# Kernel optimization log

Hardware: AMD Instinct MI355X
Metric: run time of the kernel (lower is better)

## Reference

```python
import jax, jax.numpy as jnp
import numpy as np
from math import factorial

N_ATOM = 32768
NODE_DIM = 128
HID = 64
MUL = 16          # hidden multiplicity per irrep
INS = [(0,0,0),(0,2,2),(1,1,0),(1,1,1),(1,1,2),(2,0,2),(2,2,0),(2,2,1),(2,2,2)]  # (l1,l2,l_out)
W_NUMEL = len(INS)*MUL*MUL  # 2304 per-sample tp weights

# ---------- real Clebsch-Gordan coefficients (e3nn-style, Frobenius-normalized) ----------
def _su2_cg(j1,j2,j3,m1,m2,m3):
    if m3 != m1+m2 or not (abs(j1-j2) <= j3 <= j1+j2):
        return 0.0
    f = factorial
    pref = np.sqrt((2*j3+1)*f(j3+j1-j2)*f(j3-j1+j2)*f(j1+j2-j3)/f(j1+j2+j3+1))
    pref *= np.sqrt(f(j3+m3)*f(j3-m3)*f(j1-m1)*f(j1+m1)*f(j2-m2)*f(j2+m2))
    s = 0.0
    for v in range(max(0, j2-j3-m1, j1-j3+m2), min(j1+j2-j3, j1-m1, j2+m2)+1):
        s += (-1)**v/(f(v)*f(j1+j2-j3-v)*f(j1-m1-v)*f(j2+m2-v)*f(j3-j2+m1+v)*f(j3-j1-m2+v))
    return pref*s

def _r2c(l):
    q = np.zeros((2*l+1,2*l+1), dtype=complex)
    for m in range(-l, 0):
        q[l+m, l+abs(m)] = 1/np.sqrt(2); q[l+m, l-abs(m)] = -1j/np.sqrt(2)
    q[l, l] = 1.0
    for m in range(1, l+1):
        q[l+m, l+abs(m)] = (-1)**m/np.sqrt(2); q[l+m, l-abs(m)] = 1j*(-1)**m/np.sqrt(2)
    return (-1j)**l * q

def real_cg(l1, l2, l3):
    C = np.zeros((2*l1+1,2*l2+1,2*l3+1), dtype=complex)
    for m1 in range(-l1, l1+1):
        for m2 in range(-l2, l2+1):
            m3 = m1+m2
            if abs(m3) <= l3:
                C[l1+m1, l2+m2, l3+m3] = _su2_cg(l1,l2,l3,m1,m2,m3)
    Cr = np.einsum('ij,kl,nm,ikn->jlm', _r2c(l1), _r2c(l2), np.conj(_r2c(l3)), C)
    re, im = np.real(Cr), np.imag(Cr)
    out = re if np.linalg.norm(re) >= np.linalg.norm(im) else im
    return (out / np.linalg.norm(out)).astype(np.float32)

_CG = {ins: real_cg(*ins) for ins in set(INS)}
# change of basis: irreps 1x0e+1x1e+1x2e (dim 9) -> cartesian 3x3 rank-2 tensor
_QF = np.concatenate([np.sqrt(2*l+1)*real_cg(l,1,1) for l in range(3)], 0).reshape(9,9).astype(np.float32)
_PERM = np.array([2,0,1])  # e3nn (y,z,x) -> cartesian (x,y,z)


def setup_inputs() -> dict:
    key = jax.random.key(0)
    ks = jax.random.split(key, 12)
    n = lambda k, s: jax.random.normal(k, s, dtype=jnp.float32)
    return {
        "x_scalar": n(ks[0], (N_ATOM, NODE_DIM)),
        "x_spherical": n(ks[1], (N_ATOM, 128 + 64*3 + 32*5)),
        "w_pre0": n(ks[2], (128, MUL)),
        "w_pre1": n(ks[3], (64, MUL)),
        "w_pre2": n(ks[4], (32, MUL)),
        "gw1": n(ks[5], (NODE_DIM, HID)) / float(np.sqrt(NODE_DIM)),
        "gb1": jnp.zeros((HID,), jnp.float32),
        "gw2": n(ks[6], (HID, W_NUMEL)) / float(np.sqrt(HID)),
        "gb2": jnp.zeros((W_NUMEL,), jnp.float32),
        "wpost0": n(ks[7], (3*MUL, 1)),
        "wpost1": n(ks[8], (2*MUL, 1)),
        "wpost2": n(ks[9], (4*MUL, 1)),
    }


def reference(x_scalar, x_spherical, w_pre0, w_pre1, w_pre2, gw1, gb1, gw2, gb2, wpost0, wpost1, wpost2):
    N = x_scalar.shape[0]
    # split edge irreps 128x0e + 64x1o + 32x2e
    x0 = x_spherical[:, :128]
    x1 = x_spherical[:, 128:320].reshape(N, 64, 3)
    x2 = x_spherical[:, 320:].reshape(N, 32, 5)
    # pre o3.Linear (per-l channel mixing, fan-in normalized)
    h = [
        (x0 @ w_pre0)[:, :, None] / float(np.sqrt(128.0)),              # [N,16,1] 0e
        jnp.einsum('num,uv->nvm', x1, w_pre1) / float(np.sqrt(64.0)),    # [N,16,3] 1o
        jnp.einsum('num,uv->nvm', x2, w_pre2) / float(np.sqrt(32.0)),    # [N,16,5] 2e
    ]
    # gate MLP -> per-sample tp weights [N, n_ins, u, w]
    g = (jax.nn.silu(x_scalar @ gw1 + gb1) @ gw2 + gb2).reshape(N, len(INS), MUL, MUL)
    # 'uuw' CG tensor product
    outs = {0: [], 1: [], 2: []}
    inv_sqrt_mul = float(1.0 / np.sqrt(MUL))
    for idx, (i, j, lo) in enumerate(INS):
        C = jnp.asarray(_CG[(i, j, lo)])
        o = jnp.einsum('nuw,abm,nua,nub->nwm', g[:, idx], C, h[i], h[j]) * inv_sqrt_mul
        outs[lo].append(o)
    # post o3.Linear: (48x0e + 32x1e + 64x2e) -> 1x0e + 1x1e + 1x2e
    wpost = [wpost0, wpost1, wpost2]
    ys = []
    for lo in range(3):
        z = jnp.concatenate(outs[lo], axis=1)                       # [N, n_paths*MUL, 2lo+1]
        y = jnp.einsum('num,uv->nvm', z, wpost[lo]) / float(np.sqrt(z.shape[1]))
        ys.append(y.reshape(N, 2*lo+1))
    atom_out = jnp.concatenate(ys, axis=1)                           # [N,9]
    # change of basis to cartesian rank-2 tensor + axis reindexing
    res = (atom_out @ jnp.asarray(_QF)).reshape(N, 3, 3)
    return res[:, _PERM][:, :, _PERM]
```

## Files before the change

kernel.cpp:

```cpp
#include <hip/hip_runtime.h>

#define NA 32768

typedef float  f32x4  __attribute__((ext_vector_type(4)));
typedef __bf16 bf16x8 __attribute__((ext_vector_type(8)));
typedef unsigned short u16x8 __attribute__((ext_vector_type(8)));
typedef unsigned short u16x4 __attribute__((ext_vector_type(4)));


__device__ __forceinline__ unsigned short bf16u(float f) {
    unsigned int x = __float_as_uint(f);
    x += 0x7FFFu + ((x >> 16) & 1u);
    return (unsigned short)(x >> 16);
}

__device__ __forceinline__ f32x4 MFMA16(u16x8 a, u16x8 b, f32x4 c) {
    return __builtin_amdgcn_mfma_f32_16x16x32_bf16(
        __builtin_bit_cast(bf16x8, a), __builtin_bit_cast(bf16x8, b), c, 0, 0, 0);
}

__global__ void setup_kernel(const float* __restrict__ gw1,
                             const float* __restrict__ gw2, const float* __restrict__ gb2,
                             const float* __restrict__ w_pre0, const float* __restrict__ w_pre1,
                             const float* __restrict__ w_pre2,
                             const float* __restrict__ wpost0, const float* __restrict__ wpost1,
                             const float* __restrict__ wpost2,
                             unsigned short* __restrict__ wsS, float* __restrict__ b2p)
{
    const int t = blockIdx.x * 256 + threadIdx.x;
    const int LO[9]  = {0,2,0,1,2,2,0,1,2};
    const int POS[9] = {0,0,1,0,1,2,2,1,3};
    const float SCALE[3] = {0.036084391824351615f,
                            0.04419417382415922f,
                            0.03125f};
    if (t < 8192) {
        const int j = t & 7, lane = (t >> 3) & 63, kt = (t >> 9) & 3, ct = t >> 11;
        const int k = kt * 32 + ((lane >> 4) & 3) * 8 + j;
        const int n = ct * 16 + (lane & 15);
        wsS[t] = bf16u(gw1[k * 64 + n]);
    } else if (t < 17408) {
        const int q = t - 8192;
        const int j = q & 7, lane = (q >> 3) & 63, kt = (q >> 9) & 1, ct = q >> 10;
        const int k = kt * 32 + ((lane >> 4) & 3) * 8 + j;
        const int idx = ct, u = lane & 15;
        const int lo = LO[idx];
        const float* wp = (lo == 0) ? wpost0 : (lo == 1) ? wpost1 : wpost2;
        const float* wv = wp + POS[idx] * 16;
        const float* gsrc = gw2 + (size_t)k * 2304 + idx * 256 + u * 16;
        float s = 0.f;
        for (int w = 0; w < 16; ++w) s = fmaf(gsrc[w], wv[w], s);
        wsS[8192 + q] = bf16u(s * SCALE[lo]);
    } else if (t < 19456) {
        const int q = t - 17408;
        const int j = q & 7, lane = (q >> 3) & 63, kt = q >> 9;
        const int k = kt * 32 + ((lane >> 4) & 3) * 8 + j;
        wsS[17408 + q] = bf16u(w_pre0[k * 16 + (lane & 15)] * 0.08838834764831845f);
    } else if (t < 20480) {
        const int q = t - 19456;
        const int j = q & 7, lane = (q >> 3) & 63, kt = q >> 9;
        const int k = kt * 32 + ((lane >> 4) & 3) * 8 + j;
        wsS[19456 + q] = bf16u(w_pre1[k * 16 + (lane & 15)] * 0.125f);
    } else if (t < 20992) {
        const int q = t - 20480;
        const int j = q & 7, lane = (q >> 3) & 63;
        const int k = ((lane >> 4) & 3) * 8 + j;
        wsS[20480 + q] = bf16u(w_pre2[k * 16 + (lane & 15)] * 0.17677669529663687f);
    } else if (t < 21136) {
        const int e = t - 20992;
        const int idx = e >> 4, u = e & 15;
        const int lo = LO[idx];
        const float* wp = (lo == 0) ? wpost0 : (lo == 1) ? wpost1 : wpost2;
        const float* wv = wp + POS[idx] * 16;
        const float* bsrc = gb2 + idx * 256 + u * 16;
        float sb = 0.f;
        for (int w = 0; w < 16; ++w) sb = fmaf(bsrc[w], wv[w], sb);
        b2p[e] = sb * SCALE[lo];
    }
}

__global__ __launch_bounds__(256) void csc_kernel(
    const float* __restrict__ x_scalar, const float* __restrict__ x_sph,
    const float* __restrict__ gb1,
    const unsigned short* __restrict__ wsS, const float* __restrict__ b2p,
    float* __restrict__ out)
{
    __shared__ __align__(16) unsigned short sSph[4][16][356];
    __shared__ __align__(16) unsigned short sH[4][16][72];

    const int lane = threadIdx.x & 63;
    const int wvi  = threadIdx.x >> 6;
    const int lm = lane & 15, lg = lane >> 4;
    const int n0 = (blockIdx.x * 4 + wvi) * 16;

    {
        const int a = lane >> 2, qd = lane & 3;
        const float* __restrict__ src = x_sph + (size_t)(n0 + a) * 480 + 128;
        unsigned short* dst = &sSph[wvi][a][0];
#pragma unroll
        for (int c = 0; c < 22; ++c) {
            const int i4 = qd + 4 * c;
            const float4 v = *(const float4*)(src + i4 * 4);
            u16x4 w = { bf16u(v.x), bf16u(v.y), bf16u(v.z), bf16u(v.w) };
            *(u16x4*)(dst + i4 * 4) = w;
        }
    }

    f32x4 accA0, accA1, accA2, accA3;
    {
        const float b0 = gb1[lm], b1 = gb1[16 + lm], bv2 = gb1[32 + lm], b3 = gb1[48 + lm];
        accA0 = (f32x4){b0,b0,b0,b0}; accA1 = (f32x4){b1,b1,b1,b1};
        accA2 = (f32x4){bv2,bv2,bv2,bv2}; accA3 = (f32x4){b3,b3,b3,b3};
    }
#pragma unroll
    for (int kt = 0; kt < 4; ++kt) {
        const float* xr = x_scalar + (size_t)(n0 + lm) * 128 + kt * 32 + lg * 8;
        const float4 xa = *(const float4*)xr;
        const float4 xb = *(const float4*)(xr + 4);
        const u16x8 af = { bf16u(xa.x), bf16u(xa.y), bf16u(xa.z), bf16u(xa.w),
                           bf16u(xb.x), bf16u(xb.y), bf16u(xb.z), bf16u(xb.w) };
        accA0 = MFMA16(af, *(const u16x8*)(wsS + (size_t)((0*4+kt)*64+lane)*8), accA0);
        accA1 = MFMA16(af, *(const u16x8*)(wsS + (size_t)((1*4+kt)*64+lane)*8), accA1);
        accA2 = MFMA16(af, *(const u16x8*)(wsS + (size_t)((2*4+kt)*64+lane)*8), accA2);
        accA3 = MFMA16(af, *(const u16x8*)(wsS + (size_t)((3*4+kt)*64+lane)*8), accA3);
    }
#pragma unroll
    for (int r = 0; r < 4; ++r) {
        const int atom = lg * 4 + r;
        const float v0 = accA0[r], v1 = accA1[r], v2 = accA2[r], v3 = accA3[r];
        sH[wvi][atom][ 0 + lm] = bf16u(v0 / (1.f + __expf(-v0)));
        sH[wvi][atom][16 + lm] = bf16u(v1 / (1.f + __expf(-v1)));
        sH[wvi][atom][32 + lm] = bf16u(v2 / (1.f + __expf(-v2)));
        sH[wvi][atom][48 + lm] = bf16u(v3 / (1.f + __expf(-v3)));
    }

    const u16x8 hf0 = *(const u16x8*)&sH[wvi][lm][lg * 8];
    const u16x8 hf1 = *(const u16x8*)&sH[wvi][lm][32 + lg * 8];
    f32x4 gB0, gB1, gB2, gB4, gB5, gB6, gB8;
#define INITB(ACC, CT) { const float b = b2p[(CT)*16 + lm]; ACC = (f32x4){b,b,b,b}; }
    INITB(gB0,0) INITB(gB1,1) INITB(gB2,2) INITB(gB4,4) INITB(gB5,5) INITB(gB6,6) INITB(gB8,8)
#define DOB(ACC, CT) \
    ACC = MFMA16(hf0, *(const u16x8*)(wsS + 8192 + (size_t)(((CT)*2+0)*64+lane)*8), ACC); \
    ACC = MFMA16(hf1, *(const u16x8*)(wsS + 8192 + (size_t)(((CT)*2+1)*64+lane)*8), ACC);
    DOB(gB0,0) DOB(gB1,1) DOB(gB2,2) DOB(gB4,4) DOB(gB5,5) DOB(gB6,6) DOB(gB8,8)

    f32x4 acc0 = (f32x4){0.f,0.f,0.f,0.f};
#pragma unroll
    for (int kt = 0; kt < 4; ++kt) {
        const float* xr = x_sph + (size_t)(n0 + lm) * 480 + kt * 32 + lg * 8;
        const float4 xa = *(const float4*)xr;
        const float4 xb = *(const float4*)(xr + 4);
        const u16x8 af = { bf16u(xa.x), bf16u(xa.y), bf16u(xa.z), bf16u(xa.w),
                           bf16u(xb.x), bf16u(xb.y), bf16u(xb.z), bf16u(xb.w) };
        acc0 = MFMA16(af, *(const u16x8*)(wsS + 17408 + (size_t)(kt*64+lane)*8), acc0);
    }
    const unsigned short* sp1 = &sSph[wvi][lm][0];
    f32x4 accP[3];
#pragma unroll
    for (int m = 0; m < 3; ++m) {
        f32x4 acc = (f32x4){0.f,0.f,0.f,0.f};
#pragma unroll
        for (int kt = 0; kt < 2; ++kt) {
            const int base = 3 * (kt * 32 + lg * 8) + m;
            const u16x8 af = { sp1[base], sp1[base+3], sp1[base+6],  sp1[base+9],
                               sp1[base+12], sp1[base+15], sp1[base+18], sp1[base+21] };
            acc = MFMA16(af, *(const u16x8*)(wsS + 19456 + (size_t)(kt*64+lane)*8), acc);
        }
        accP[m] = acc;
    }
    const unsigned short* sp2 = &sSph[wvi][lm][192];
    f32x4 accQ[5];
#pragma unroll
    for (int m = 0; m < 5; ++m) {
        const int base = 5 * (lg * 8) + m;
        const u16x8 af = { sp2[base], sp2[base+5], sp2[base+10], sp2[base+15],
                           sp2[base+20], sp2[base+25], sp2[base+30], sp2[base+35] };
        accQ[m] = MFMA16(af, *(const u16x8*)(wsS + 20480 + (size_t)lane*8),
                         (f32x4){0.f,0.f,0.f,0.f});
    }

    const float C110 = 0.5773502691896258f;
    const float C220 = 0.4472135954999579f;
    const float Ca = 0.31622776601683794f, Cb = 0.18257418583505536f;
    const float A2 = 0.2390457218668787f, B2c = 0.20701966780270626f, D2 = 0.11952286093343936f;
    const float is3 = 0.5773502691896258f, is6 = 0.4082482904638631f, is2 = 0.7071067811865476f;

#pragma unroll
    for (int r = 0; r < 4; ++r) {
        const float h0 = acc0[r];
        const float p0 = accP[0][r], p1 = accP[1][r], p2 = accP[2][r];
        const float q0 = accQ[0][r], q1 = accQ[1][r], q2 = accQ[2][r],
                    q3 = accQ[3][r], q4 = accQ[4][r];
        const float G0 = gB0[r], G1 = gB1[r], G2 = gB2[r], G4 = gB4[r],
                    G5 = gB5[r], G6 = gB6[r], G8 = gB8[r];

        float y0 = G0 * h0 * h0
                 + G2 * C110 * (p0*p0 + p1*p1 + p2*p2)
                 + G6 * C220 * (q0*q0 + q1*q1 + q2*q2 + q3*q3 + q4*q4);
        float z0, z1, z2, z3, z4;
        {
            const float c15 = C220 * h0 * (G1 + G5);
            z0 = c15 * q0; z1 = c15 * q1; z2 = c15 * q2; z3 = c15 * q3; z4 = c15 * q4;
        }
        z0 = fmaf(G4, 2.f*Ca*p0*p2, z0);
        z1 = fmaf(G4, 2.f*Ca*p0*p1, z1);
        z2 = fmaf(G4, Cb*(2.f*p1*p1 - p0*p0 - p2*p2), z2);
        z3 = fmaf(G4, 2.f*Ca*p2*p1, z3);
        z4 = fmaf(G4, Ca*(p2*p2 - p0*p0), z4);
        z0 = fmaf(G8, -2.f*A2*q0*q2 + 2.f*B2c*q1*q3, z0);
        z1 = fmaf(G8,  2.f*B2c*(q0*q3 - q4*q1) + 2.f*D2*q1*q2, z1);
        z2 = fmaf(G8,  A2*(q2*q2 - q0*q0 - q4*q4) + D2*(q1*q1 + q3*q3), z2);
        z3 = fmaf(G8,  2.f*B2c*(q0*q1 + q3*q4) + 2.f*D2*q2*q3, z3);
        z4 = fmaf(G8, -2.f*A2*q2*q4 + B2c*(q3*q3 - q1*q1), z4);

#pragma unroll
        for (int msk = 1; msk <= 8; msk <<= 1) {
            y0 += __shfl_xor(y0, msk, 64);
            z0 += __shfl_xor(z0, msk, 64);
            z1 += __shfl_xor(z1, msk, 64);
            z2 += __shfl_xor(z2, msk, 64);
            z3 += __shfl_xor(z3, msk, 64);
            z4 += __shfl_xor(z4, msk, 64);
        }

        const float c0 = y0*is3 - z2*is6 - z4*is2;
        const float c4 = y0*is3 + 2.f*z2*is6;
        const float c8 = y0*is3 - z2*is6 + z4*is2;
        const float c1 = z1*is2, c2v = z0*is2, c5 = z3*is2;
        if (lm < 9) {
            const float val = (lm==0)?c8 : (lm==1)?c2v : (lm==2)?c5 : (lm==3)?c2v
                            : (lm==4)?c0 : (lm==5)?c1 : (lm==6)?c5 : (lm==7)?c1 : c4;
            out[(size_t)(n0 + lg*4 + r) * 9 + lm] = val;
        }
    }
}

extern "C" void kernel_launch(void* const* d_in, const int* in_sizes, int n_in,
                              void* d_out, int out_size, void* d_ws, size_t ws_size,
                              hipStream_t stream) {
    const float* x_scalar = (const float*)d_in[0];
    const float* x_sph    = (const float*)d_in[1];
    const float* w_pre0   = (const float*)d_in[2];
    const float* w_pre1   = (const float*)d_in[3];
    const float* w_pre2   = (const float*)d_in[4];
    const float* gw1      = (const float*)d_in[5];
    const float* gb1      = (const float*)d_in[6];
    const float* gw2      = (const float*)d_in[7];
    const float* gb2      = (const float*)d_in[8];
    const float* wpost0   = (const float*)d_in[9];
    const float* wpost1   = (const float*)d_in[10];
    const float* wpost2   = (const float*)d_in[11];

    unsigned short* wsS = (unsigned short*)d_ws;
    float* b2p = (float*)((char*)d_ws + 41984);

    setup_kernel<<<83, 256, 0, stream>>>(gw1, gw2, gb2, w_pre0, w_pre1, w_pre2,
                                         wpost0, wpost1, wpost2, wsS, b2p);
    csc_kernel<<<512, 256, 0, stream>>>(x_scalar, x_sph, gb1, wsS, b2p, (float*)d_out);
}
```

Baseline: 27.56 us.

## Split gate MLP and spherical projection across two waves per 16-atom block

Each block now handles 16 atoms with two waves. Wave 0 computes the gate MLP and tensor-product weights and writes them to shared memory, while wave 1 loads and deinterleaves the spherical inputs into per-component LDS tiles so MFMA fragments come from single vector reads. Float-to-bf16 conversion switches to the native cast. This shortens the per-wave dependency chain and removes the strided scalar LDS gathers, at the cost of a block barrier, extra LDS traffic for the gate values, and four times as many blocks.

```diff
diff --git a/kernel.cpp b/kernel.cpp
--- a/kernel.cpp
+++ b/kernel.cpp
@@ -5,7 +5,6 @@
 typedef float  f32x4  __attribute__((ext_vector_type(4)));
 typedef __bf16 bf16x8 __attribute__((ext_vector_type(8)));
 typedef unsigned short u16x8 __attribute__((ext_vector_type(8)));
-typedef unsigned short u16x4 __attribute__((ext_vector_type(4)));
 
 
 __device__ __forceinline__ unsigned short bf16u(float f) {
@@ -13,7 +12,9 @@
     x += 0x7FFFu + ((x >> 16) & 1u);
     return (unsigned short)(x >> 16);
 }
-
+__device__ __forceinline__ unsigned short cvt1(float f) {
+    return __builtin_bit_cast(unsigned short, (__bf16)f);
+}
 __device__ __forceinline__ f32x4 MFMA16(u16x8 a, u16x8 b, f32x4 c) {
     return __builtin_amdgcn_mfma_f32_16x16x32_bf16(
         __builtin_bit_cast(bf16x8, a), __builtin_bit_cast(bf16x8, b), c, 0, 0, 0);
@@ -78,70 +79,99 @@
     }
 }
 
-__global__ __launch_bounds__(256) void csc_kernel(
+__global__ __launch_bounds__(128, 3) void csc_kernel(
     const float* __restrict__ x_scalar, const float* __restrict__ x_sph,
     const float* __restrict__ gb1,
     const unsigned short* __restrict__ wsS, const float* __restrict__ b2p,
     float* __restrict__ out)
 {
-    __shared__ __align__(16) unsigned short sSph[4][16][356];
-    __shared__ __align__(16) unsigned short sH[4][16][72];
+    __shared__ __align__(16) unsigned short sH[16][72];
+    __shared__ __align__(16) unsigned short sT1[3][16][72];
+    __shared__ __align__(16) unsigned short sT2[5][16][40];
+    __shared__ float sG[7 * 16 * 17];
 
     const int lane = threadIdx.x & 63;
-    const int wvi  = threadIdx.x >> 6;
+    const int wv   = threadIdx.x >> 6;
     const int lm = lane & 15, lg = lane >> 4;
-    const int n0 = (blockIdx.x * 4 + wvi) * 16;
+    const int n0 = blockIdx.x * 16;
+
+    if (wv == 0) {
+        f32x4 accA0, accA1, accA2, accA3;
+        {
+            const float b0 = gb1[lm], b1 = gb1[16 + lm], bv2 = gb1[32 + lm], b3 = gb1[48 + lm];
+            accA0 = (f32x4){b0,b0,b0,b0}; accA1 = (f32x4){b1,b1,b1,b1};
+            accA2 = (f32x4){bv2,bv2,bv2,bv2}; accA3 = (f32x4){b3,b3,b3,b3};
+        }
+#pragma unroll
+        for (int kt = 0; kt < 4; ++kt) {
+            const float* xr = x_scalar + (size_t)(n0 + lm) * 128 + kt * 32 + lg * 8;
+            const float4 xa = *(const float4*)xr;
+            const float4 xb = *(const float4*)(xr + 4);
+            const u16x8 af = { cvt1(xa.x), cvt1(xa.y), cvt1(xa.z), cvt1(xa.w),
+                               cvt1(xb.x), cvt1(xb.y), cvt1(xb.z), cvt1(xb.w) };
+            accA0 = MFMA16(af, *(const u16x8*)(wsS + (size_t)((0*4+kt)*64+lane)*8), accA0);
+            accA1 = MFMA16(af, *(const u16x8*)(wsS + (size_t)((1*4+kt)*64+lane)*8), accA1);
+            accA2 = MFMA16(af, *(const u16x8*)(wsS + (size_t)((2*4+kt)*64+lane)*8), accA2);
+            accA3 = MFMA16(af, *(const u16x8*)(wsS + (size_t)((3*4+kt)*64+lane)*8), accA3);
+        }
+#pragma unroll
+        for (int r = 0; r < 4; ++r) {
+            const int atom = lg * 4 + r;
+            const float v0 = accA0[r], v1 = accA1[r], v2 = accA2[r], v3 = accA3[r];
+            sH[atom][ 0 + lm] = cvt1(v0 / (1.f + __expf(-v0)));
+            sH[atom][16 + lm] = cvt1(v1 / (1.f + __expf(-v1)));
+            sH[atom][32 + lm] = cvt1(v2 / (1.f + __expf(-v2)));
+            sH[atom][48 + lm] = cvt1(v3 / (1.f + __expf(-v3)));
+        }
+
+        const u16x8 hf0 = *(const u16x8*)&sH[lm][lg * 8];
+        const u16x8 hf1 = *(const u16x8*)&sH[lm][32 + lg * 8];
+        f32x4 gB0, gB1, gB2, gB4, gB5, gB6, gB8;
+#define INITB(ACC, CT) { const float b = b2p[(CT)*16 + lm]; ACC = (f32x4){b,b,b,b}; }
+        INITB(gB0,0) INITB(gB1,1) INITB(gB2,2) INITB(gB4,4) INITB(gB5,5) INITB(gB6,6) INITB(gB8,8)
+#define DOB(ACC, CT) \
+        ACC = MFMA16(hf0, *(const u16x8*)(wsS + 8192 + (size_t)(((CT)*2+0)*64+lane)*8), ACC); \
+        ACC = MFMA16(hf1, *(const u16x8*)(wsS + 8192 + (size_t)(((CT)*2+1)*64+lane)*8), ACC);
+        DOB(gB0,0) DOB(gB1,1) DOB(gB2,2) DOB(gB4,4) DOB(gB5,5) DOB(gB6,6) DOB(gB8,8)
+
+#define WRG(ACC, CI) { _Pragma("unroll") \
+        for (int r = 0; r < 4; ++r) sG[((CI)*16 + lg*4 + r)*17 + lm] = ACC[r]; }
+        WRG(gB0,0) WRG(gB1,1) WRG(gB2,2) WRG(gB4,3) WRG(gB5,4) WRG(gB6,5) WRG(gB8,6)
+
+        __syncthreads();
+        return;
+    }
 
     {
-        const int a = lane >> 2, qd = lane & 3;
-        const float* __restrict__ src = x_sph + (size_t)(n0 + a) * 480 + 128;
-        unsigned short* dst = &sSph[wvi][a][0];
-#pragma unroll
-        for (int c = 0; c < 22; ++c) {
-            const int i4 = qd + 4 * c;
-            const float4 v = *(const float4*)(src + i4 * 4);
-            u16x4 w = { bf16u(v.x), bf16u(v.y), bf16u(v.z), bf16u(v.w) };
-            *(u16x4*)(dst + i4 * 4) = w;
-        }
-    }
-
-    f32x4 accA0, accA1, accA2, accA3;
-    {
-        const float b0 = gb1[lm], b1 = gb1[16 + lm], bv2 = gb1[32 + lm], b3 = gb1[48 + lm];
-        accA0 = (f32x4){b0,b0,b0,b0}; accA1 = (f32x4){b1,b1,b1,b1};
-        accA2 = (f32x4){bv2,bv2,bv2,bv2}; accA3 = (f32x4){b3,b3,b3,b3};
-    }
-#pragma unroll
-    for (int kt = 0; kt < 4; ++kt) {
-        const float* xr = x_scalar + (size_t)(n0 + lm) * 128 + kt * 32 + lg * 8;
-        const float4 xa = *(const float4*)xr;
-        const float4 xb = *(const float4*)(xr + 4);
-        const u16x8 af = { bf16u(xa.x), bf16u(xa.y), bf16u(xa.z), bf16u(xa.w),
-                           bf16u(xb.x), bf16u(xb.y), bf16u(xb.z), bf16u(xb.w) };
-        accA0 = MFMA16(af, *(const u16x8*)(wsS + (size_t)((0*4+kt)*64+lane)*8), accA0);
-        accA1 = MFMA16(af, *(const u16x8*)(wsS + (size_t)((1*4+kt)*64+lane)*8), accA1);
-        accA2 = MFMA16(af, *(const u16x8*)(wsS + (size_t)((2*4+kt)*64+lane)*8), accA2);
-        accA3 = MFMA16(af, *(const u16x8*)(wsS + (size_t)((3*4+kt)*64+lane)*8), accA3);
-    }
-#pragma unroll
-    for (int r = 0; r < 4; ++r) {
-        const int atom = lg * 4 + r;
-        const float v0 = accA0[r], v1 = accA1[r], v2 = accA2[r], v3 = accA3[r];
-        sH[wvi][atom][ 0 + lm] = bf16u(v0 / (1.f + __expf(-v0)));
-        sH[wvi][atom][16 + lm] = bf16u(v1 / (1.f + __expf(-v1)));
-        sH[wvi][atom][32 + lm] = bf16u(v2 / (1.f + __expf(-v2)));
-        sH[wvi][atom][48 + lm] = bf16u(v3 / (1.f + __expf(-v3)));
-    }
-
-    const u16x8 hf0 = *(const u16x8*)&sH[wvi][lm][lg * 8];
-    const u16x8 hf1 = *(const u16x8*)&sH[wvi][lm][32 + lg * 8];
-    f32x4 gB0, gB1, gB2, gB4, gB5, gB6, gB8;
-#define INITB(ACC, CT) { const float b = b2p[(CT)*16 + lm]; ACC = (f32x4){b,b,b,b}; }
-    INITB(gB0,0) INITB(gB1,1) INITB(gB2,2) INITB(gB4,4) INITB(gB5,5) INITB(gB6,6) INITB(gB8,8)
-#define DOB(ACC, CT) \
-    ACC = MFMA16(hf0, *(const u16x8*)(wsS + 8192 + (size_t)(((CT)*2+0)*64+lane)*8), ACC); \
-    ACC = MFMA16(hf1, *(const u16x8*)(wsS + 8192 + (size_t)(((CT)*2+1)*64+lane)*8), ACC);
-    DOB(gB0,0) DOB(gB1,1) DOB(gB2,2) DOB(gB4,4) DOB(gB5,5) DOB(gB6,6) DOB(gB8,8)
+        const int a = lane >> 2, q = lane & 3;
+        const float* rowp = x_sph + (size_t)(n0 + a) * 480;
+        float F1[48];
+        const float* s1 = rowp + 128 + q * 48;
+#pragma unroll
+        for (int c = 0; c < 12; ++c) *(float4*)&F1[c * 4] = *(const float4*)(s1 + c * 4);
+#pragma unroll
+        for (int m = 0; m < 3; ++m) {
+            u16x8 w0, w1;
+#pragma unroll
+            for (int j = 0; j < 8; ++j) {
+                w0[j] = cvt1(F1[3 * j + m]);
+                w1[j] = cvt1(F1[24 + 3 * j + m]);
+            }
+            *(u16x8*)&sT1[m][a][q * 16]     = w0;
+            *(u16x8*)&sT1[m][a][q * 16 + 8] = w1;
+        }
+        float F2[40];
+        const float* s2 = rowp + 320 + q * 40;
+#pragma unroll
+        for (int c = 0; c < 10; ++c) *(float4*)&F2[c * 4] = *(const float4*)(s2 + c * 4);
+#pragma unroll
+        for (int m = 0; m < 5; ++m) {
+            u16x8 w;
+#pragma unroll
+            for (int j = 0; j < 8; ++j) w[j] = cvt1(F2[5 * j + m]);
+            *(u16x8*)&sT2[m][a][q * 8] = w;
+        }
+    }
 
     f32x4 acc0 = (f32x4){0.f,0.f,0.f,0.f};
 #pragma unroll
@@ -149,34 +179,30 @@
         const float* xr = x_sph + (size_t)(n0 + lm) * 480 + kt * 32 + lg * 8;
         const float4 xa = *(const float4*)xr;
         const float4 xb = *(const float4*)(xr + 4);
-        const u16x8 af = { bf16u(xa.x), bf16u(xa.y), bf16u(xa.z), bf16u(xa.w),
-                           bf16u(xb.x), bf16u(xb.y), bf16u(xb.z), bf16u(xb.w) };
+        const u16x8 af = { cvt1(xa.x), cvt1(xa.y), cvt1(xa.z), cvt1(xa.w),
+                           cvt1(xb.x), cvt1(xb.y), cvt1(xb.z), cvt1(xb.w) };
         acc0 = MFMA16(af, *(const u16x8*)(wsS + 17408 + (size_t)(kt*64+lane)*8), acc0);
     }
-    const unsigned short* sp1 = &sSph[wvi][lm][0];
     f32x4 accP[3];
 #pragma unroll
     for (int m = 0; m < 3; ++m) {
         f32x4 acc = (f32x4){0.f,0.f,0.f,0.f};
 #pragma unroll
         for (int kt = 0; kt < 2; ++kt) {
-            const int base = 3 * (kt * 32 + lg * 8) + m;
-            const u16x8 af = { sp1[base], sp1[base+3], sp1[base+6],  sp1[base+9],
-                               sp1[base+12], sp1[base+15], sp1[base+18], sp1[base+21] };
+            const u16x8 af = *(const u16x8*)&sT1[m][lm][kt * 32 + lg * 8];
             acc = MFMA16(af, *(const u16x8*)(wsS + 19456 + (size_t)(kt*64+lane)*8), acc);
         }
         accP[m] = acc;
     }
-    const unsigned short* sp2 = &sSph[wvi][lm][192];
     f32x4 accQ[5];
 #pragma unroll
     for (int m = 0; m < 5; ++m) {
-        const int base = 5 * (lg * 8) + m;
-        const u16x8 af = { sp2[base], sp2[base+5], sp2[base+10], sp2[base+15],
-                           sp2[base+20], sp2[base+25], sp2[base+30], sp2[base+35] };
+        const u16x8 af = *(const u16x8*)&sT2[m][lm][lg * 8];
         accQ[m] = MFMA16(af, *(const u16x8*)(wsS + 20480 + (size_t)lane*8),
                          (f32x4){0.f,0.f,0.f,0.f});
     }
+
+    __syncthreads();
 
     const float C110 = 0.5773502691896258f;
     const float C220 = 0.4472135954999579f;
@@ -186,12 +212,19 @@
 
 #pragma unroll
     for (int r = 0; r < 4; ++r) {
+        const int row = lg * 4 + r;
+        const float G0 = sG[(0*16 + row)*17 + lm];
+        const float G1 = sG[(1*16 + row)*17 + lm];
+        const float G2 = sG[(2*16 + row)*17 + lm];
+        const float G4 = sG[(3*16 + row)*17 + lm];
+        const float G5 = sG[(4*16 + row)*17 + lm];
+        const float G6 = sG[(5*16 + row)*17 + lm];
+        const float G8 = sG[(6*16 + row)*17 + lm];
+
         const float h0 = acc0[r];
         const float p0 = accP[0][r], p1 = accP[1][r], p2 = accP[2][r];
         const float q0 = accQ[0][r], q1 = accQ[1][r], q2 = accQ[2][r],
                     q3 = accQ[3][r], q4 = accQ[4][r];
-        const float G0 = gB0[r], G1 = gB1[r], G2 = gB2[r], G4 = gB4[r],
-                    G5 = gB5[r], G6 = gB6[r], G8 = gB8[r];
 
         float y0 = G0 * h0 * h0
                  + G2 * C110 * (p0*p0 + p1*p1 + p2*p2)
@@ -229,7 +262,7 @@
         if (lm < 9) {
             const float val = (lm==0)?c8 : (lm==1)?c2v : (lm==2)?c5 : (lm==3)?c2v
                             : (lm==4)?c0 : (lm==5)?c1 : (lm==6)?c5 : (lm==7)?c1 : c4;
-            out[(size_t)(n0 + lg*4 + r) * 9 + lm] = val;
+            out[(size_t)(n0 + row) * 9 + lm] = val;
         }
     }
 }
@@ -255,5 +288,5 @@
 
     setup_kernel<<<83, 256, 0, stream>>>(gw1, gw2, gb2, w_pre0, w_pre1, w_pre2,
                                          wpost0, wpost1, wpost2, wsS, b2p);
-    csc_kernel<<<512, 256, 0, stream>>>(x_scalar, x_sph, gb1, wsS, b2p, (float*)d_out);
-}
+    csc_kernel<<<NA / 16, 128, 0, stream>>>(x_scalar, x_sph, gb1, wsS, b2p, (float*)d_out);
+}
```

Result: slower. 31.07 us (+12.7%).

## Load spherical features straight into registers and drop the LDS staging buffer

Applied to the files above, without the earlier changes.

Each lane now loads its own slice of the l=0/1/2 spherical features from global memory into registers and builds the MFMA A-fragments by gathering strided elements in registers. This removes the shared-memory staging array, the scattered LDS reads, and a second global read of the l=0 block. It also swaps the manual round-to-nearest bf16 conversion for the compiler's native bf16 cast, which may map to hardware conversion instructions. The cost is higher register pressure from about 120 floats held per lane, which could reduce occupancy.

```diff
diff --git a/kernel.cpp b/kernel.cpp
--- a/kernel.cpp
+++ b/kernel.cpp
@@ -5,7 +5,6 @@
 typedef float  f32x4  __attribute__((ext_vector_type(4)));
 typedef __bf16 bf16x8 __attribute__((ext_vector_type(8)));
 typedef unsigned short u16x8 __attribute__((ext_vector_type(8)));
-typedef unsigned short u16x4 __attribute__((ext_vector_type(4)));
 
 
 __device__ __forceinline__ unsigned short bf16u(float f) {
@@ -13,7 +12,9 @@
     x += 0x7FFFu + ((x >> 16) & 1u);
     return (unsigned short)(x >> 16);
 }
-
+__device__ __forceinline__ unsigned short cvt1(float f) {
+    return __builtin_bit_cast(unsigned short, (__bf16)f);
+}
 __device__ __forceinline__ f32x4 MFMA16(u16x8 a, u16x8 b, f32x4 c) {
     return __builtin_amdgcn_mfma_f32_16x16x32_bf16(
         __builtin_bit_cast(bf16x8, a), __builtin_bit_cast(bf16x8, b), c, 0, 0, 0);
@@ -84,7 +85,6 @@
     const unsigned short* __restrict__ wsS, const float* __restrict__ b2p,
     float* __restrict__ out)
 {
-    __shared__ __align__(16) unsigned short sSph[4][16][356];
     __shared__ __align__(16) unsigned short sH[4][16][72];
 
     const int lane = threadIdx.x & 63;
@@ -92,18 +92,41 @@
     const int lm = lane & 15, lg = lane >> 4;
     const int n0 = (blockIdx.x * 4 + wvi) * 16;
 
-    {
-        const int a = lane >> 2, qd = lane & 3;
-        const float* __restrict__ src = x_sph + (size_t)(n0 + a) * 480 + 128;
-        unsigned short* dst = &sSph[wvi][a][0];
-#pragma unroll
-        for (int c = 0; c < 22; ++c) {
-            const int i4 = qd + 4 * c;
-            const float4 v = *(const float4*)(src + i4 * 4);
-            u16x4 w = { bf16u(v.x), bf16u(v.y), bf16u(v.z), bf16u(v.w) };
-            *(u16x4*)(dst + i4 * 4) = w;
-        }
-    }
+    const float* __restrict__ rowq = x_sph + (size_t)(n0 + lm) * 480;
+
+    float S0[32], S1[48], S2[40];
+#pragma unroll
+    for (int kt = 0; kt < 4; ++kt) {
+        *(float4*)&S0[kt * 8]     = *(const float4*)(rowq + kt * 32 + lg * 8);
+        *(float4*)&S0[kt * 8 + 4] = *(const float4*)(rowq + kt * 32 + lg * 8 + 4);
+    }
+#pragma unroll
+    for (int kt = 0; kt < 2; ++kt)
+#pragma unroll
+        for (int c = 0; c < 6; ++c)
+            *(float4*)&S1[kt * 24 + c * 4] =
+                *(const float4*)(rowq + 128 + 96 * kt + 24 * lg + c * 4);
+#pragma unroll
+    for (int c = 0; c < 10; ++c)
+        *(float4*)&S2[c * 4] = *(const float4*)(rowq + 320 + 40 * lg + c * 4);
+
+    u16x8 f0[4];
+#pragma unroll
+    for (int kt = 0; kt < 4; ++kt)
+#pragma unroll
+        for (int j = 0; j < 8; ++j) f0[kt][j] = cvt1(S0[kt * 8 + j]);
+    u16x8 f1[3][2];
+#pragma unroll
+    for (int m = 0; m < 3; ++m)
+#pragma unroll
+        for (int kt = 0; kt < 2; ++kt)
+#pragma unroll
+            for (int j = 0; j < 8; ++j) f1[m][kt][j] = cvt1(S1[kt * 24 + 3 * j + m]);
+    u16x8 f2[5];
+#pragma unroll
+    for (int m = 0; m < 5; ++m)
+#pragma unroll
+        for (int j = 0; j < 8; ++j) f2[m][j] = cvt1(S2[5 * j + m]);
 
     f32x4 accA0, accA1, accA2, accA3;
     {
@@ -116,8 +139,8 @@
         const float* xr = x_scalar + (size_t)(n0 + lm) * 128 + kt * 32 + lg * 8;
         const float4 xa = *(const float4*)xr;
         const float4 xb = *(const float4*)(xr + 4);
-        const u16x8 af = { bf16u(xa.x), bf16u(xa.y), bf16u(xa.z), bf16u(xa.w),
-                           bf16u(xb.x), bf16u(xb.y), bf16u(xb.z), bf16u(xb.w) };
+        const u16x8 af = { cvt1(xa.x), cvt1(xa.y), cvt1(xa.z), cvt1(xa.w),
+                           cvt1(xb.x), cvt1(xb.y), cvt1(xb.z), cvt1(xb.w) };
         accA0 = MFMA16(af, *(const u16x8*)(wsS + (size_t)((0*4+kt)*64+lane)*8), accA0);
         accA1 = MFMA16(af, *(const u16x8*)(wsS + (size_t)((1*4+kt)*64+lane)*8), accA1);
         accA2 = MFMA16(af, *(const u16x8*)(wsS + (size_t)((2*4+kt)*64+lane)*8), accA2);
@@ -127,10 +150,10 @@
     for (int r = 0; r < 4; ++r) {
         const int atom = lg * 4 + r;
         const float v0 = accA0[r], v1 = accA1[r], v2 = accA2[r], v3 = accA3[r];
-        sH[wvi][atom][ 0 + lm] = bf16u(v0 / (1.f + __expf(-v0)));
-        sH[wvi][atom][16 + lm] = bf16u(v1 / (1.f + __expf(-v1)));
-        sH[wvi][atom][32 + lm] = bf16u(v2 / (1.f + __expf(-v2)));
-        sH[wvi][atom][48 + lm] = bf16u(v3 / (1.f + __expf(-v3)));
+        sH[wvi][atom][ 0 + lm] = cvt1(v0 / (1.f + __expf(-v0)));
+        sH[wvi][atom][16 + lm] = cvt1(v1 / (1.f + __expf(-v1)));
+        sH[wvi][atom][32 + lm] = cvt1(v2 / (1.f + __expf(-v2)));
+        sH[wvi][atom][48 + lm] = cvt1(v3 / (1.f + __expf(-v3)));
     }
 
     const u16x8 hf0 = *(const u16x8*)&sH[wvi][lm][lg * 8];
@@ -145,38 +168,22 @@
 
     f32x4 acc0 = (f32x4){0.f,0.f,0.f,0.f};
 #pragma unroll
-    for (int kt = 0; kt < 4; ++kt) {
-        const float* xr = x_sph + (size_t)(n0 + lm) * 480 + kt * 32 + lg * 8;
-        const float4 xa = *(const float4*)xr;
-        const float4 xb = *(const float4*)(xr + 4);
-        const u16x8 af = { bf16u(xa.x), bf16u(xa.y), bf16u(xa.z), bf16u(xa.w),
-                           bf16u(xb.x), bf16u(xb.y), bf16u(xb.z), bf16u(xb.w) };
-        acc0 = MFMA16(af, *(const u16x8*)(wsS + 17408 + (size_t)(kt*64+lane)*8), acc0);
-    }
-    const unsigned short* sp1 = &sSph[wvi][lm][0];
+    for (int kt = 0; kt < 4; ++kt)
+        acc0 = MFMA16(f0[kt], *(const u16x8*)(wsS + 17408 + (size_t)(kt*64+lane)*8), acc0);
     f32x4 accP[3];
 #pragma unroll
     for (int m = 0; m < 3; ++m) {
         f32x4 acc = (f32x4){0.f,0.f,0.f,0.f};
 #pragma unroll
-        for (int kt = 0; kt < 2; ++kt) {
-            const int base = 3 * (kt * 32 + lg * 8) + m;
-            const u16x8 af = { sp1[base], sp1[base+3], sp1[base+6],  sp1[base+9],
-                               sp1[base+12], sp1[base+15], sp1[base+18], sp1[base+21] };
-            acc = MFMA16(af, *(const u16x8*)(wsS + 19456 + (size_t)(kt*64+lane)*8), acc);
-        }
+        for (int kt = 0; kt < 2; ++kt)
+            acc = MFMA16(f1[m][kt], *(const u16x8*)(wsS + 19456 + (size_t)(kt*64+lane)*8), acc);
         accP[m] = acc;
     }
-    const unsigned short* sp2 = &sSph[wvi][lm][192];
     f32x4 accQ[5];
 #pragma unroll
-    for (int m = 0; m < 5; ++m) {
-        const int base = 5 * (lg * 8) + m;
-        const u16x8 af = { sp2[base], sp2[base+5], sp2[base+10], sp2[base+15],
-                           sp2[base+20], sp2[base+25], sp2[base+30], sp2[base+35] };
-        accQ[m] = MFMA16(af, *(const u16x8*)(wsS + 20480 + (size_t)lane*8),
+    for (int m = 0; m < 5; ++m)
+        accQ[m] = MFMA16(f2[m], *(const u16x8*)(wsS + 20480 + (size_t)lane*8),
                          (f32x4){0.f,0.f,0.f,0.f});
-    }
 
     const float C110 = 0.5773502691896258f;
     const float C220 = 0.4472135954999579f;
@@ -186,6 +193,7 @@
 
 #pragma unroll
     for (int r = 0; r < 4; ++r) {
+        const int row = lg * 4 + r;
         const float h0 = acc0[r];
         const float p0 = accP[0][r], p1 = accP[1][r], p2 = accP[2][r];
         const float q0 = accQ[0][r], q1 = accQ[1][r], q2 = accQ[2][r],
@@ -229,7 +237,7 @@
         if (lm < 9) {
             const float val = (lm==0)?c8 : (lm==1)?c2v : (lm==2)?c5 : (lm==3)?c2v
                             : (lm==4)?c0 : (lm==5)?c1 : (lm==6)?c5 : (lm==7)?c1 : c4;
-            out[(size_t)(n0 + lg*4 + r) * 9 + lm] = val;
+            out[(size_t)(n0 + row) * 9 + lm] = val;
         }
     }
 }
@@ -255,5 +263,5 @@
 
     setup_kernel<<<83, 256, 0, stream>>>(gw1, gw2, gb2, w_pre0, w_pre1, w_pre2,
                                          wpost0, wpost1, wpost2, wsS, b2p);
-    csc_kernel<<<512, 256, 0, stream>>>(x_scalar, x_sph, gb1, wsS, b2p, (float*)d_out);
-}
+    csc_kernel<<<NA / 64, 256, 0, stream>>>(x_scalar, x_sph, gb1, wsS, b2p, (float*)d_out);
+}
```

Measured after the change: 29.33 us. +6.4%, slower.
